# Kernel tuning notes

Hardware: AMD Instinct MI355X
Metric: run time of the kernel (lower is better)

## Reference

```python
import jax, jax.numpy as jnp
import numpy as np

SCALE = 65536          # Q16.16 fixed point, matching the torch module's SCALE
N_SEGMENTS = 16


def setup_inputs() -> dict:
    key = jax.random.key(0)
    k1, k2, k3, k4, k5 = jax.random.split(key, 5)
    # Large activation tensor -> memory-bound elementwise bucketize+affine.
    x = jax.random.normal(k1, (32, 4096, 1024), dtype=jnp.float32) * 2.0
    # n_segments-1 interior breakpoints, sorted, Q16.16 covering ~[-4, 4].
    breakpoints = jnp.sort(
        jax.random.randint(k2, (N_SEGMENTS - 1,), -4 * SCALE, 4 * SCALE, dtype=jnp.int32)
    )
    # Per-segment intercepts in Q16.16, within +/- 1.0 real units.
    intercepts = jax.random.randint(k3, (N_SEGMENTS,), -SCALE, SCALE, dtype=jnp.int32)
    # Per-segment slope signs in {-1, +1}.
    signs = 2 * jax.random.randint(k4, (N_SEGMENTS,), 0, 2, dtype=jnp.int32) - 1
    # Per-segment slope exponents: slope magnitude = 2^-exp (arithmetic right shift).
    exps = jax.random.randint(k5, (N_SEGMENTS,), 0, 8, dtype=jnp.int32)
    return {
        "x": x,
        "breakpoints": breakpoints,
        "intercepts": intercepts,
        "signs": signs,
        "exps": exps,
    }


def _plac_int32(x_q16, breakpoints, intercepts, signs, exps):
    # Bucketize each Q16.16 element against the sorted interior breakpoints;
    # seg in [0, n_segments-1].
    seg = jnp.searchsorted(breakpoints, x_q16, side="right").astype(jnp.int32)
    b = jnp.take(intercepts, seg)   # segment intercept (Q16.16)
    s = jnp.take(signs, seg)        # segment sign (+/-1)
    e = jnp.take(exps, seg)         # segment slope exponent
    # y = intercept + sign * (x >> exp) in int32 Q16.16 (arithmetic shift).
    return b + s * jnp.right_shift(x_q16, e)


def reference(x, breakpoints, intercepts, signs, exps):
    # Faithful to torch forward: detach, quantize to Q16.16 int32, eval, dequantize.
    x_q16 = (jax.lax.stop_gradient(x).astype(jnp.float32) * SCALE).astype(jnp.int32)
    y_q16 = _plac_int32(x_q16, breakpoints, intercepts, signs, exps)
    return (y_q16.astype(jnp.float32) / SCALE).astype(x.dtype)
```

## Files before the change

### kernel.cpp

```cpp
#include <hip/hip_runtime.h>
#include <limits.h>
#include <math.h>

#define NSEG 16
#define LMAX 2048

typedef float f32x4 __attribute__((ext_vector_type(4)));
typedef float f32x2 __attribute__((ext_vector_type(2)));

__device__ __forceinline__ float plac_tail(float t, f32x4 c) {
    float u = floorf(t * c.z);
    return fmaf(c.y, u, c.x);
}

__device__ __forceinline__ float plac_lut_one(float xv, const f32x2* __restrict__ s_lut,
                                              const f32x4* __restrict__ s_tab,
                                              int LOm, int S, int Lm1) {
    float t = truncf(xv * 65536.0f);
    int xq = (int)t;
    int idx = (xq - LOm) >> S;
    idx = min(max(idx, 0), Lm1);
    f32x2 e = s_lut[idx];
    int m = __float_as_int(e.y);
    int seg = m + (t >= e.x ? 1 : 0);
    return plac_tail(t, s_tab[seg]);
}

__device__ __forceinline__ float plac_full_one(float xv, const float* __restrict__ bpf,
                                               const f32x4* __restrict__ s_tab) {
    float t = truncf(xv * 65536.0f);
    int seg = 0;
    #pragma unroll
    for (int k = 0; k < 15; ++k) seg += (t >= bpf[k]);
    return plac_tail(t, s_tab[seg]);
}

__global__ __launch_bounds__(256, 8) void plac_kernel(
    const float* __restrict__ x,
    const int* __restrict__ bps,
    const int* __restrict__ intercepts,
    const int* __restrict__ signs,
    const int* __restrict__ exps,
    float* __restrict__ out,
    long long n4, long long n)
{
    __shared__ f32x2 s_lut[LMAX];
    __shared__ f32x4 s_tab[NSEG];

    const int tid = threadIdx.x;

    int bp[15];
    #pragma unroll
    for (int k = 0; k < 15; ++k) bp[k] = bps[k];
    int gapmin = INT_MAX;
    #pragma unroll
    for (int k = 0; k < 14; ++k) gapmin = min(gapmin, bp[k + 1] - bp[k]);
    const int LO = bp[0];
    const int range = bp[14] - bp[0];
    int Smin = 0;
    while (((range >> Smin) + 2) > LMAX) ++Smin;
    int S = 0;
    bool valid = false;
    if (gapmin > 0) {
        S = 31 - __clz(gapmin);
        valid = (S >= Smin);
    }
    const int L   = (range >> S) + 2;
    const int Lm1 = L - 1;
    const int LOm = LO - (1 << S);

    if (tid < NSEG) {
        float b  = (float)intercepts[tid] * (1.0f / 65536.0f);
        float s  = (float)signs[tid]      * (1.0f / 65536.0f);
        float ei = __int_as_float((127 - exps[tid]) << 23);
        f32x4 row = {b, s, ei, 0.0f};
        s_tab[tid] = row;
    }

    if (valid) {
        for (int i = tid; i < L; i += 256) {
            int m = 0;
            float bpn = INFINITY;
            if (i > 0) {
                int left = LO + ((i - 1) << S);
                #pragma unroll
                for (int k = 14; k >= 0; --k) {
                    if (bp[k] <= left) m += 1;
                    else               bpn = (float)bp[k];
                }
            } else {
                bpn = (float)bp[0];
            }
            f32x2 e = {bpn, __int_as_float(m)};
            s_lut[i] = e;
        }
    }
    __syncthreads();

    const f32x4* __restrict__ x4 = (const f32x4*)x;
    f32x4* __restrict__ o4 = (f32x4*)out;
    long long i0     = (long long)blockIdx.x * blockDim.x + tid;
    long long stride = (long long)gridDim.x * blockDim.x;

    if (valid) {
        for (long long i = i0; i < n4; i += stride) {
            f32x4 v = x4[i];
            f32x4 r;
            #pragma unroll
            for (int j = 0; j < 4; ++j)
                r[j] = plac_lut_one(v[j], s_lut, s_tab, LOm, S, Lm1);
            o4[i] = r;
        }
        if (blockIdx.x == 0) {
            for (long long ii = n4 * 4 + tid; ii < n; ii += blockDim.x)
                out[ii] = plac_lut_one(x[ii], s_lut, s_tab, LOm, S, Lm1);
        }
    } else {
        float bpf[15];
        #pragma unroll
        for (int k = 0; k < 15; ++k) bpf[k] = (float)bp[k];
        for (long long i = i0; i < n4; i += stride) {
            f32x4 v = x4[i];
            f32x4 r;
            #pragma unroll
            for (int j = 0; j < 4; ++j)
                r[j] = plac_full_one(v[j], bpf, s_tab);
            o4[i] = r;
        }
        if (blockIdx.x == 0) {
            for (long long ii = n4 * 4 + tid; ii < n; ii += blockDim.x)
                out[ii] = plac_full_one(x[ii], bpf, s_tab);
        }
    }
}

extern "C" void kernel_launch(void* const* d_in, const int* in_sizes, int n_in,
                              void* d_out, int out_size, void* d_ws, size_t ws_size,
                              hipStream_t stream) {
    const float* x          = (const float*)d_in[0];
    const int*   bps        = (const int*)d_in[1];
    const int*   intercepts = (const int*)d_in[2];
    const int*   signs      = (const int*)d_in[3];
    const int*   exps       = (const int*)d_in[4];
    float* out = (float*)d_out;

    long long n  = (long long)out_size;
    long long n4 = n / 4;

    const int block = 256;
    long long blocks_needed = (n4 + block - 1) / block;
    if (blocks_needed < 1) blocks_needed = 1;
    int grid = (int)((blocks_needed < 2048) ? blocks_needed : 2048);

    plac_kernel<<<grid, block, 0, stream>>>(x, bps, intercepts, signs, exps,
                                            out, n4, n);
}
```

Before: 211.1 us.

## Use contiguous per-block chunks with 2x unrolled loads and a smaller grid

Work is split so each of 512 blocks handles one contiguous chunk of float4s instead of a grid-stride loop over 2048 blocks. The main loop issues two independent 16-byte loads per thread per iteration to raise memory-level parallelism, and the launch bounds drop the minimum-occupancy hint. The aim is to cut per-block LUT setup overhead and improve streaming locality, at the risk of fewer waves in flight to hide latency and tail imbalance across blocks.

```diff
diff --git a/kernel.cpp b/kernel.cpp
--- a/kernel.cpp
+++ b/kernel.cpp
@@ -35,14 +35,14 @@
     return plac_tail(t, s_tab[seg]);
 }
 
-__global__ __launch_bounds__(256, 8) void plac_kernel(
+__global__ __launch_bounds__(256) void plac_kernel(
     const float* __restrict__ x,
     const int* __restrict__ bps,
     const int* __restrict__ intercepts,
     const int* __restrict__ signs,
     const int* __restrict__ exps,
     float* __restrict__ out,
-    long long n4, long long n)
+    long long n4, long long n, long long per)
 {
     __shared__ f32x2 s_lut[LMAX];
     __shared__ f32x4 s_tab[NSEG];
@@ -76,7 +76,6 @@
         f32x4 row = {b, s, ei, 0.0f};
         s_tab[tid] = row;
     }
-
     if (valid) {
         for (int i = tid; i < L; i += 256) {
             int m = 0;
@@ -99,36 +98,60 @@
 
     const f32x4* __restrict__ x4 = (const f32x4*)x;
     f32x4* __restrict__ o4 = (f32x4*)out;
-    long long i0     = (long long)blockIdx.x * blockDim.x + tid;
-    long long stride = (long long)gridDim.x * blockDim.x;
+
+    long long start = (long long)blockIdx.x * per;
+    long long end   = start + per;
+    if (end > n4) end = n4;
 
     if (valid) {
-        for (long long i = i0; i < n4; i += stride) {
+        long long p = start;
+        for (; p + 512 <= end; p += 512) {
+            f32x4 v0 = x4[p + tid];
+            f32x4 v1 = x4[p + 256 + tid];
+            f32x4 r0, r1;
+            #pragma unroll
+            for (int j = 0; j < 4; ++j) r0[j] = plac_lut_one(v0[j], s_lut, s_tab, LOm, S, Lm1);
+            #pragma unroll
+            for (int j = 0; j < 4; ++j) r1[j] = plac_lut_one(v1[j], s_lut, s_tab, LOm, S, Lm1);
+            o4[p + tid]       = r0;
+            o4[p + 256 + tid] = r1;
+        }
+        for (long long i = p + tid; i < end; i += 256) {
             f32x4 v = x4[i];
             f32x4 r;
             #pragma unroll
-            for (int j = 0; j < 4; ++j)
-                r[j] = plac_lut_one(v[j], s_lut, s_tab, LOm, S, Lm1);
+            for (int j = 0; j < 4; ++j) r[j] = plac_lut_one(v[j], s_lut, s_tab, LOm, S, Lm1);
             o4[i] = r;
         }
         if (blockIdx.x == 0) {
-            for (long long ii = n4 * 4 + tid; ii < n; ii += blockDim.x)
+            for (long long ii = n4 * 4 + tid; ii < n; ii += 256)
                 out[ii] = plac_lut_one(x[ii], s_lut, s_tab, LOm, S, Lm1);
         }
     } else {
         float bpf[15];
         #pragma unroll
         for (int k = 0; k < 15; ++k) bpf[k] = (float)bp[k];
-        for (long long i = i0; i < n4; i += stride) {
+        long long p = start;
+        for (; p + 512 <= end; p += 512) {
+            f32x4 v0 = x4[p + tid];
+            f32x4 v1 = x4[p + 256 + tid];
+            f32x4 r0, r1;
+            #pragma unroll
+            for (int j = 0; j < 4; ++j) r0[j] = plac_full_one(v0[j], bpf, s_tab);
+            #pragma unroll
+            for (int j = 0; j < 4; ++j) r1[j] = plac_full_one(v1[j], bpf, s_tab);
+            o4[p + tid]       = r0;
+            o4[p + 256 + tid] = r1;
+        }
+        for (long long i = p + tid; i < end; i += 256) {
             f32x4 v = x4[i];
             f32x4 r;
             #pragma unroll
-            for (int j = 0; j < 4; ++j)
-                r[j] = plac_full_one(v[j], bpf, s_tab);
+            for (int j = 0; j < 4; ++j) r[j] = plac_full_one(v[j], bpf, s_tab);
             o4[i] = r;
         }
         if (blockIdx.x == 0) {
-            for (long long ii = n4 * 4 + tid; ii < n; ii += blockDim.x)
+            for (long long ii = n4 * 4 + tid; ii < n; ii += 256)
                 out[ii] = plac_full_one(x[ii], bpf, s_tab);
         }
     }
@@ -147,11 +170,9 @@
     long long n  = (long long)out_size;
     long long n4 = n / 4;
 
-    const int block = 256;
-    long long blocks_needed = (n4 + block - 1) / block;
-    if (blocks_needed < 1) blocks_needed = 1;
-    int grid = (int)((blocks_needed < 2048) ? blocks_needed : 2048);
+    const int grid = 512;
+    long long per = (n4 + grid - 1) / grid;
 
-    plac_kernel<<<grid, block, 0, stream>>>(x, bps, intercepts, signs, exps,
-                                            out, n4, n);
+    plac_kernel<<<grid, 256, 0, stream>>>(x, bps, intercepts, signs, exps,
+                                          out, n4, n, per);
 }
```

After: 208.9 us. About the same (-1.0%).
